# Optimization experiments

Hardware: AMD Instinct MI355X
Metric: run time of the kernel (lower is better)

Reference implementation:

```python
import jax, jax.numpy as jnp
import numpy as np

N = 100000      # nodes (max(content_indices)+1)
E = 1600000     # edges
TXT, VIS = 768, 512
IN = 128        # in_channels (already even)
FEAT = IN + 3   # feature_size = in_channels + 3 (ars)
HID, OUT, CAT = 128, 128, 2
NEG_SLOPE = 0.2


def setup_inputs() -> dict:
    key = jax.random.key(0)
    ks = jax.random.split(key, 20)
    p = lambda k, sh: jax.random.normal(k, sh, jnp.float32) * 0.02
    return {
        "image_features": jax.random.normal(ks[0], (N, VIS), jnp.float32),
        "text_features": jax.random.normal(ks[1], (N, TXT), jnp.float32),
        "content_indices": jnp.arange(N, dtype=jnp.int32),
        "gt_indices": jax.random.randint(ks[2], (N,), 0, 2, jnp.int32),
        "edges": jax.random.randint(ks[3], (E, 2), 0, N, jnp.int32),
        "ars": jax.random.uniform(ks[4], (N, 3), jnp.float32),
        # linear projections
        "Wi": p(ks[5], (VIS, IN // 2)), "bi": jnp.zeros((IN // 2,), jnp.float32),
        "Wt": p(ks[6], (TXT, IN // 2)), "bt": jnp.zeros((IN // 2,), jnp.float32),
        # GATConv layer 0: FEAT -> HID (heads=1)
        "W0": p(ks[7], (FEAT, HID)), "as0": p(ks[8], (HID,)), "ad0": p(ks[9], (HID,)),
        "b0": jnp.zeros((HID,), jnp.float32),
        # GATConv layer 1: HID -> OUT
        "W1": p(ks[10], (HID, OUT)), "as1": p(ks[11], (OUT,)), "ad1": p(ks[12], (OUT,)),
        "b1": jnp.zeros((OUT,), jnp.float32),
        "Wa": p(ks[13], (OUT, CAT)), "ba": jnp.zeros((CAT,), jnp.float32),
        "Wd": p(ks[14], (OUT, CAT)), "bd": jnp.zeros((CAT,), jnp.float32),
    }


def gat_conv(x, src, dst, W, att_src, att_dst, bias):
    """PyG GATConv, heads=1, add_self_loops=True, negative_slope=0.2."""
    h = x @ W                                    # [N, D]
    loop = jnp.arange(N, dtype=src.dtype)
    s = jnp.concatenate([src, loop])             # [E+N]
    d = jnp.concatenate([dst, loop])
    a_s = (h * att_src).sum(-1)                  # [N]
    a_d = (h * att_dst).sum(-1)
    e = jax.nn.leaky_relu(a_s[s] + a_d[d], NEG_SLOPE)   # [E+N]
    # segment softmax over incoming edges of each dst node
    e_max = jax.ops.segment_max(e, d, num_segments=N)
    ee = jnp.exp(e - e_max[d])
    denom = jax.ops.segment_sum(ee, d, num_segments=N)
    alpha = ee / (denom[d] + 1e-16)
    out = jax.ops.segment_sum(h[s] * alpha[:, None], d, num_segments=N)
    return out + bias


def reference(image_features, text_features, content_indices, gt_indices, edges, ars,
              Wi, bi, Wt, bt, W0, as0, ad0, b0, W1, as1, ad1, b1, Wa, ba, Wd, bd):
    img = image_features @ Wi + bi              # [N, IN//2]
    txt = text_features @ Wt + bt               # [N, IN//2]
    inp = jnp.concatenate([img, txt, ars], axis=1)   # [N, FEAT]
    node = jnp.zeros((N, FEAT), jnp.float32).at[content_indices].set(inp)
    node = jax.nn.gelu(node, approximate=False)
    src, dst = edges[:, 0], edges[:, 1]         # edge_index = edges.T
    h = gat_conv(node, src, dst, W0, as0, ad0, b0)
    h = jax.nn.relu(h)                          # PyG GAT inter-layer act
    h = gat_conv(h, src, dst, W1, as1, ad1, b1)
    out = jax.nn.gelu(h, approximate=False)     # [N, OUT]
    angles = out @ Wa + ba                      # [N, CAT]
    dists = out @ Wd + bd
    # per-edge tiny dot products (bmm of [E,1,C] x [E,C,1])
    ap = jnp.sum(angles[src] * angles[dst], axis=-1, keepdims=True)  # [E,1]
    dp = jnp.sum(dists[src] * dists[dst], axis=-1, keepdims=True)
    prediction = jnp.concatenate([ap, dp], axis=-1)   # [E, 2]
    return out, prediction
```

## Files before the change

kernel.cpp:

```cpp
#include <hip/hip_runtime.h>
#include <math.h>

#define N_NODES 100000
#define N_EDGES 1600000
#define FEAT 131
#define HID 128

__device__ __forceinline__ float geluf(float x) {
    return 0.5f * x * (1.0f + erff(x * 0.7071067811865475f));
}
__device__ __forceinline__ float leakyf(float x) {
    return x >= 0.0f ? x : 0.2f * x;
}
__device__ __forceinline__ float wave_reduce_max(float v) {
#pragma unroll
    for (int o = 32; o > 0; o >>= 1) v = fmaxf(v, __shfl_xor(v, o, 64));
    return v;
}
__device__ __forceinline__ float wave_reduce_sum(float v) {
#pragma unroll
    for (int o = 32; o > 0; o >>= 1) v += __shfl_xor(v, o, 64);
    return v;
}

template <int ACT>
__global__ __launch_bounds__(256) void gemm_tiled(
    const float* __restrict__ A, int lda, int M, int K,
    const float* __restrict__ B, int ldb,
    const float* __restrict__ bias,
    float* __restrict__ C, int ldc, int colOff,
    const int* __restrict__ rowIdx)
{
    __shared__ float As[16][68];
    __shared__ float Bs[16][64];
    int tid = threadIdx.x;
    int m0 = blockIdx.x * 64;
    int n0 = blockIdx.y * 64;
    int tx = tid & 15, ty = tid >> 4;
    float acc[4][4] = {};

    for (int k0 = 0; k0 < K; k0 += 16) {
#pragma unroll
        for (int i = 0; i < 4; ++i) {
            int idx = tid + i * 256;
            int r = idx >> 4, kk = idx & 15;
            int row = m0 + r, k = k0 + kk;
            As[kk][r] = (row < M && k < K) ? A[(size_t)row * lda + k] : 0.0f;
        }
#pragma unroll
        for (int i = 0; i < 4; ++i) {
            int idx = tid + i * 256;
            int kk = idx >> 6, c = idx & 63;
            int k = k0 + kk;
            Bs[kk][c] = (k < K) ? B[(size_t)k * ldb + n0 + c] : 0.0f;
        }
        __syncthreads();
#pragma unroll
        for (int kk = 0; kk < 16; ++kk) {
            float4 a4 = *(const float4*)&As[kk][ty * 4];
            float4 b4 = *(const float4*)&Bs[kk][tx * 4];
            float av[4] = {a4.x, a4.y, a4.z, a4.w};
            float bv[4] = {b4.x, b4.y, b4.z, b4.w};
#pragma unroll
            for (int i = 0; i < 4; ++i)
#pragma unroll
                for (int j = 0; j < 4; ++j)
                    acc[i][j] = fmaf(av[i], bv[j], acc[i][j]);
        }
        __syncthreads();
    }

#pragma unroll
    for (int i = 0; i < 4; ++i) {
        int row = m0 + ty * 4 + i;
        if (row >= M) continue;
        int orow = rowIdx ? rowIdx[row] : row;
#pragma unroll
        for (int j = 0; j < 4; ++j) {
            int c = n0 + tx * 4 + j;
            float v = acc[i][j];
            if (bias) v += bias[c];
            if (ACT == 1) v = geluf(v);
            C[(size_t)orow * ldc + colOff + c] = v;
        }
    }
}

__global__ void ars_kernel(const float* __restrict__ ars, const int* __restrict__ ci,
                           float* __restrict__ node)
{
    int i = blockIdx.x * blockDim.x + threadIdx.x;
    if (i >= N_NODES * 3) return;
    int n = i / 3, j = i - n * 3;
    node[(size_t)ci[n] * FEAT + 128 + j] = geluf(ars[i]);
}

__global__ void hist_dst(const int* __restrict__ edges, int* __restrict__ deg)
{
    int e = blockIdx.x * blockDim.x + threadIdx.x;
    if (e < N_EDGES) atomicAdd(&deg[edges[2 * e + 1]], 1);
}

__global__ __launch_bounds__(1024) void scan_excl(const int* __restrict__ deg,
                                                  int* __restrict__ row_ptr)
{
    __shared__ int sd[1024];
    int tid = threadIdx.x;
    int base = 0;
    for (int start = 0; start < N_NODES; start += 1024) {
        int i = start + tid;
        int v = (i < N_NODES) ? deg[i] : 0;
        sd[tid] = v;
        __syncthreads();
        for (int off = 1; off < 1024; off <<= 1) {
            int t = (tid >= off) ? sd[tid - off] : 0;
            __syncthreads();
            sd[tid] += t;
            __syncthreads();
        }
        if (i < N_NODES) row_ptr[i] = base + sd[tid] - v;
        base += sd[1023];
        __syncthreads();
    }
    if (tid == 0) row_ptr[N_NODES] = base;
}

__global__ void copy_int(const int* __restrict__ src, int* __restrict__ dst, int n)
{
    int i = blockIdx.x * blockDim.x + threadIdx.x;
    if (i < n) dst[i] = src[i];
}

__global__ void scatter_csr(const int* __restrict__ edges, int* __restrict__ cursor,
                            int* __restrict__ csr_src)
{
    int e = blockIdx.x * blockDim.x + threadIdx.x;
    if (e >= N_EDGES) return;
    int s = edges[2 * e], d = edges[2 * e + 1];
    int pos = atomicAdd(&cursor[d], 1);
    csr_src[pos] = s;
}

__global__ __launch_bounds__(256) void attn_scores(
    const float* __restrict__ h, const float* __restrict__ atts,
    const float* __restrict__ attd, float* __restrict__ as_, float* __restrict__ ad_)
{
    int lane = threadIdx.x & 63;
    int node = blockIdx.x * 4 + (threadIdx.x >> 6);
    if (node >= N_NODES) return;
    float h0 = h[(size_t)node * HID + lane];
    float h1 = h[(size_t)node * HID + 64 + lane];
    float s = h0 * atts[lane] + h1 * atts[64 + lane];
    float d = h0 * attd[lane] + h1 * attd[64 + lane];
    s = wave_reduce_sum(s);
    d = wave_reduce_sum(d);
    if (lane == 0) { as_[node] = s; ad_[node] = d; }
}

template <int ACT>
__global__ __launch_bounds__(256) void gat_aggregate(
    const float* __restrict__ h,
    const float* __restrict__ as_, const float* __restrict__ ad_,
    const int* __restrict__ row_ptr, const int* __restrict__ csr_src,
    const float* __restrict__ bias, float* __restrict__ outp)
{
    int lane = threadIdx.x & 63;
    int node = blockIdx.x * 4 + (threadIdx.x >> 6);
    if (node >= N_NODES) return;
    int start = row_ptr[node];
    int deg = row_ptr[node + 1] - start;
    float adn = ad_[node];
    float e_self = leakyf(as_[node] + adn);
    float acc0 = 0.0f, acc1 = 0.0f;
    float m, denom;

    if (deg <= 64) {
        int s = 0;
        float e = -INFINITY;
        if (lane < deg) {
            s = csr_src[start + lane];
            e = leakyf(as_[s] + adn);
        }
        m = fmaxf(wave_reduce_max(e), e_self);
        float w = (lane < deg) ? __expf(e - m) : 0.0f;
        denom = wave_reduce_sum(w) + __expf(e_self - m);
        for (int jj = 0; jj < deg; ++jj) {
            int sj = __shfl(s, jj, 64);
            float wj = __shfl(w, jj, 64);
            acc0 += wj * h[(size_t)sj * HID + lane];
            acc1 += wj * h[(size_t)sj * HID + 64 + lane];
        }
    } else {
        float lm = -INFINITY;
        for (int j = lane; j < deg; j += 64)
            lm = fmaxf(lm, leakyf(as_[csr_src[start + j]] + adn));
        m = fmaxf(wave_reduce_max(lm), e_self);
        float lsum = 0.0f;
        for (int j = lane; j < deg; j += 64)
            lsum += __expf(leakyf(as_[csr_src[start + j]] + adn) - m);
        denom = wave_reduce_sum(lsum) + __expf(e_self - m);
        for (int c0 = 0; c0 < deg; c0 += 64) {
            int j = c0 + lane;
            int s = 0;
            float w = 0.0f;
            if (j < deg) {
                s = csr_src[start + j];
                w = __expf(leakyf(as_[s] + adn) - m);
            }
            int cnt = min(64, deg - c0);
            for (int jj = 0; jj < cnt; ++jj) {
                int sj = __shfl(s, jj, 64);
                float wj = __shfl(w, jj, 64);
                acc0 += wj * h[(size_t)sj * HID + lane];
                acc1 += wj * h[(size_t)sj * HID + 64 + lane];
            }
        }
    }

    float wself = __expf(e_self - m);
    acc0 = (acc0 + wself * h[(size_t)node * HID + lane]) / denom;
    acc1 = (acc1 + wself * h[(size_t)node * HID + 64 + lane]) / denom;
    acc0 += bias[lane];
    acc1 += bias[64 + lane];
    if (ACT == 0) {
        acc0 = fmaxf(acc0, 0.0f);
        acc1 = fmaxf(acc1, 0.0f);
    } else {
        acc0 = geluf(acc0);
        acc1 = geluf(acc1);
    }
    outp[(size_t)node * HID + lane] = acc0;
    outp[(size_t)node * HID + 64 + lane] = acc1;
}

__global__ __launch_bounds__(256) void head_proj(
    const float* __restrict__ outf,
    const float* __restrict__ Wa, const float* __restrict__ ba,
    const float* __restrict__ Wd, const float* __restrict__ bd,
    float* __restrict__ adp)
{
    int lane = threadIdx.x & 63;
    int node = blockIdx.x * 4 + (threadIdx.x >> 6);
    if (node >= N_NODES) return;
    float o0 = outf[(size_t)node * HID + lane];
    float o1 = outf[(size_t)node * HID + 64 + lane];
    float a0 = o0 * Wa[lane * 2] + o1 * Wa[(lane + 64) * 2];
    float a1 = o0 * Wa[lane * 2 + 1] + o1 * Wa[(lane + 64) * 2 + 1];
    float d0 = o0 * Wd[lane * 2] + o1 * Wd[(lane + 64) * 2];
    float d1 = o0 * Wd[lane * 2 + 1] + o1 * Wd[(lane + 64) * 2 + 1];
    a0 = wave_reduce_sum(a0);
    a1 = wave_reduce_sum(a1);
    d0 = wave_reduce_sum(d0);
    d1 = wave_reduce_sum(d1);
    if (lane == 0) {
        float4 v = make_float4(a0 + ba[0], a1 + ba[1], d0 + bd[0], d1 + bd[1]);
        ((float4*)adp)[node] = v;
    }
}

__global__ void edge_pred(const int* __restrict__ edges, const float* __restrict__ adp,
                          float* __restrict__ pred)
{
    int e = blockIdx.x * blockDim.x + threadIdx.x;
    if (e >= N_EDGES) return;
    int s = edges[2 * e], d = edges[2 * e + 1];
    float4 ps = ((const float4*)adp)[s];
    float4 pd = ((const float4*)adp)[d];
    pred[2 * e] = ps.x * pd.x + ps.y * pd.y;
    pred[2 * e + 1] = ps.z * pd.z + ps.w * pd.w;
}

extern "C" void kernel_launch(void* const* d_in, const int* in_sizes, int n_in,
                              void* d_out, int out_size, void* d_ws, size_t ws_size,
                              hipStream_t stream)
{
    const float* imgf = (const float*)d_in[0];
    const float* txtf = (const float*)d_in[1];
    const int* ci     = (const int*)d_in[2];
    const int* edges  = (const int*)d_in[4];
    const float* ars  = (const float*)d_in[5];
    const float* Wi   = (const float*)d_in[6];
    const float* bi   = (const float*)d_in[7];
    const float* Wt   = (const float*)d_in[8];
    const float* bt   = (const float*)d_in[9];
    const float* W0   = (const float*)d_in[10];
    const float* as0  = (const float*)d_in[11];
    const float* ad0  = (const float*)d_in[12];
    const float* b0   = (const float*)d_in[13];
    const float* W1   = (const float*)d_in[14];
    const float* as1  = (const float*)d_in[15];
    const float* ad1  = (const float*)d_in[16];
    const float* b1   = (const float*)d_in[17];
    const float* Wa   = (const float*)d_in[18];
    const float* ba   = (const float*)d_in[19];
    const float* Wd   = (const float*)d_in[20];
    const float* bd   = (const float*)d_in[21];
    (void)in_sizes; (void)n_in; (void)out_size; (void)ws_size;

    float* out0 = (float*)d_out;
    float* pred = out0 + (size_t)N_NODES * HID;

    char* ws = (char*)d_ws;
    size_t off = 0;
    auto alloc = [&](size_t bytes) -> void* {
        void* p = ws + off;
        off += (bytes + 255) & ~(size_t)255;
        return p;
    };
    float* node   = (float*)alloc((size_t)N_NODES * FEAT * 4);
    float* hA     = (float*)alloc((size_t)N_NODES * HID * 4);
    float* as_buf = (float*)alloc((size_t)N_NODES * 4);
    float* ad_buf = (float*)alloc((size_t)N_NODES * 4);
    int* row_ptr  = (int*)alloc((size_t)(N_NODES + 1) * 4);
    int* cursor   = (int*)alloc((size_t)N_NODES * 4);
    int* csr_src  = (int*)alloc((size_t)N_EDGES * 4);
    float* adp    = (float*)alloc((size_t)N_NODES * 4 * 4);

    int mtiles = (N_NODES + 63) / 64;
    int nwaveblocks = N_NODES / 4;

    hipMemsetAsync(cursor, 0, (size_t)N_NODES * 4, stream);
    hist_dst<<<(N_EDGES + 255) / 256, 256, 0, stream>>>(edges, cursor);
    scan_excl<<<1, 1024, 0, stream>>>(cursor, row_ptr);
    copy_int<<<(N_NODES + 255) / 256, 256, 0, stream>>>(row_ptr, cursor, N_NODES);
    scatter_csr<<<(N_EDGES + 255) / 256, 256, 0, stream>>>(edges, cursor, csr_src);

    gemm_tiled<1><<<dim3(mtiles, 1), 256, 0, stream>>>(imgf, 512, N_NODES, 512, Wi, 64, bi, node, FEAT, 0, ci);
    gemm_tiled<1><<<dim3(mtiles, 1), 256, 0, stream>>>(txtf, 768, N_NODES, 768, Wt, 64, bt, node, FEAT, 64, ci);
    ars_kernel<<<(N_NODES * 3 + 255) / 256, 256, 0, stream>>>(ars, ci, node);

    gemm_tiled<0><<<dim3(mtiles, 2), 256, 0, stream>>>(node, FEAT, N_NODES, FEAT, W0, HID, nullptr, hA, HID, 0, nullptr);
    attn_scores<<<nwaveblocks, 256, 0, stream>>>(hA, as0, ad0, as_buf, ad_buf);
    gat_aggregate<0><<<nwaveblocks, 256, 0, stream>>>(hA, as_buf, ad_buf, row_ptr, csr_src, b0, node);

    gemm_tiled<0><<<dim3(mtiles, 2), 256, 0, stream>>>(node, HID, N_NODES, HID, W1, HID, nullptr, hA, HID, 0, nullptr);
    attn_scores<<<nwaveblocks, 256, 0, stream>>>(hA, as1, ad1, as_buf, ad_buf);
    gat_aggregate<1><<<nwaveblocks, 256, 0, stream>>>(hA, as_buf, ad_buf, row_ptr, csr_src, b1, out0);

    head_proj<<<nwaveblocks, 256, 0, stream>>>(out0, Wa, ba, Wd, bd, adp);
    edge_pred<<<(N_EDGES + 255) / 256, 256, 0, stream>>>(edges, adp, pred);
}
```

Before: 1.835 ms.

## Use 128x64 register-prefetched GEMM tiles with float4 loads and padded features

Replaces the 64x64 GEMM with a 128x64 tile that computes 8x4 outputs per thread over a K-step of 32. It prefetches the next global tile into registers while the current one is computed, and uses float4 loads and stores. The node feature width is padded from 131 to 132, and W0 is zero-padded to match, so rows are 16-byte aligned for vector access. In exchange it uses more registers and shared memory per block and adds a small padding kernel.

```diff
diff --git a/kernel.cpp b/kernel.cpp
--- a/kernel.cpp
+++ b/kernel.cpp
@@ -3,7 +3,7 @@
 
 #define N_NODES 100000
 #define N_EDGES 1600000
-#define FEAT 131
+#define FEATP 132
 #define HID 128
 
 __device__ __forceinline__ float geluf(float x) {
@@ -24,45 +24,69 @@
 }
 
 template <int ACT>
-__global__ __launch_bounds__(256) void gemm_tiled(
+__global__ __launch_bounds__(256) void gemm128(
     const float* __restrict__ A, int lda, int M, int K,
     const float* __restrict__ B, int ldb,
     const float* __restrict__ bias,
     float* __restrict__ C, int ldc, int colOff,
     const int* __restrict__ rowIdx)
 {
-    __shared__ float As[16][68];
-    __shared__ float Bs[16][64];
-    int tid = threadIdx.x;
-    int m0 = blockIdx.x * 64;
-    int n0 = blockIdx.y * 64;
-    int tx = tid & 15, ty = tid >> 4;
-    float acc[4][4] = {};
-
-    for (int k0 = 0; k0 < K; k0 += 16) {
+    __shared__ float As[32][132];
+    __shared__ float Bs[32][64];
+    const int tid = threadIdx.x;
+    const int m0 = blockIdx.x * 128;
+    const int n0 = blockIdx.y * 64;
+    const int tx = tid & 15, ty = tid >> 4;
+
+    const int arow = tid >> 3;
+    const int acol = (tid & 7) * 4;
+    const int brow = tid >> 4;
+    const int bcol = (tid & 15) * 4;
+
+    float4 pa[4], pb[2];
+    const int T = (K + 31) / 32;
+
+    auto fetch = [&](int k0) {
 #pragma unroll
         for (int i = 0; i < 4; ++i) {
-            int idx = tid + i * 256;
-            int r = idx >> 4, kk = idx & 15;
-            int row = m0 + r, k = k0 + kk;
-            As[kk][r] = (row < M && k < K) ? A[(size_t)row * lda + k] : 0.0f;
-        }
+            int row = m0 + i * 32 + arow;
+            int k = k0 + acol;
+            pa[i] = (row < M && k < K) ? *(const float4*)&A[(size_t)row * lda + k]
+                                       : make_float4(0.f, 0.f, 0.f, 0.f);
+        }
+#pragma unroll
+        for (int i = 0; i < 2; ++i) {
+            int k = k0 + i * 16 + brow;
+            pb[i] = (k < K) ? *(const float4*)&B[(size_t)k * ldb + n0 + bcol]
+                            : make_float4(0.f, 0.f, 0.f, 0.f);
+        }
+    };
+
+    float acc[8][4] = {};
+    fetch(0);
+    for (int t = 0; t < T; ++t) {
 #pragma unroll
         for (int i = 0; i < 4; ++i) {
-            int idx = tid + i * 256;
-            int kk = idx >> 6, c = idx & 63;
-            int k = k0 + kk;
-            Bs[kk][c] = (k < K) ? B[(size_t)k * ldb + n0 + c] : 0.0f;
-        }
+            int row = i * 32 + arow;
+            As[acol + 0][row] = pa[i].x;
+            As[acol + 1][row] = pa[i].y;
+            As[acol + 2][row] = pa[i].z;
+            As[acol + 3][row] = pa[i].w;
+        }
+#pragma unroll
+        for (int i = 0; i < 2; ++i)
+            *(float4*)&Bs[i * 16 + brow][bcol] = pb[i];
         __syncthreads();
-#pragma unroll
-        for (int kk = 0; kk < 16; ++kk) {
-            float4 a4 = *(const float4*)&As[kk][ty * 4];
-            float4 b4 = *(const float4*)&Bs[kk][tx * 4];
-            float av[4] = {a4.x, a4.y, a4.z, a4.w};
-            float bv[4] = {b4.x, b4.y, b4.z, b4.w};
-#pragma unroll
-            for (int i = 0; i < 4; ++i)
+        if (t + 1 < T) fetch((t + 1) * 32);
+#pragma unroll
+        for (int kk = 0; kk < 32; ++kk) {
+            float4 a0 = *(const float4*)&As[kk][ty * 8];
+            float4 a1 = *(const float4*)&As[kk][ty * 8 + 4];
+            float4 b  = *(const float4*)&Bs[kk][tx * 4];
+            float av[8] = {a0.x, a0.y, a0.z, a0.w, a1.x, a1.y, a1.z, a1.w};
+            float bv[4] = {b.x, b.y, b.z, b.w};
+#pragma unroll
+            for (int i = 0; i < 8; ++i)
 #pragma unroll
                 for (int j = 0; j < 4; ++j)
                     acc[i][j] = fmaf(av[i], bv[j], acc[i][j]);
@@ -71,18 +95,20 @@
     }
 
 #pragma unroll
-    for (int i = 0; i < 4; ++i) {
-        int row = m0 + ty * 4 + i;
+    for (int i = 0; i < 8; ++i) {
+        int row = m0 + ty * 8 + i;
         if (row >= M) continue;
         int orow = rowIdx ? rowIdx[row] : row;
+        float4 v;
+        float* vp = (float*)&v;
 #pragma unroll
         for (int j = 0; j < 4; ++j) {
-            int c = n0 + tx * 4 + j;
-            float v = acc[i][j];
-            if (bias) v += bias[c];
-            if (ACT == 1) v = geluf(v);
-            C[(size_t)orow * ldc + colOff + c] = v;
-        }
+            float x = acc[i][j];
+            if (bias) x += bias[n0 + tx * 4 + j];
+            if (ACT == 1) x = geluf(x);
+            vp[j] = x;
+        }
+        *(float4*)&C[(size_t)orow * ldc + colOff + n0 + tx * 4] = v;
     }
 }
 
@@ -90,9 +116,18 @@
                            float* __restrict__ node)
 {
     int i = blockIdx.x * blockDim.x + threadIdx.x;
-    if (i >= N_NODES * 3) return;
-    int n = i / 3, j = i - n * 3;
-    node[(size_t)ci[n] * FEAT + 128 + j] = geluf(ars[i]);
+    if (i >= N_NODES * 4) return;
+    int n = i >> 2, j = i & 3;
+    float v = (j < 3) ? geluf(ars[n * 3 + j]) : 0.0f;
+    node[(size_t)ci[n] * FEATP + 128 + j] = v;
+}
+
+__global__ void pad_W0(const float* __restrict__ W0, float* __restrict__ W0p)
+{
+    int i = blockIdx.x * blockDim.x + threadIdx.x;
+    if (i >= FEATP * HID) return;
+    int r = i >> 7;
+    W0p[i] = (r < 131) ? W0[i] : 0.0f;
 }
 
 __global__ void hist_dst(const int* __restrict__ edges, int* __restrict__ deg)
@@ -307,7 +342,7 @@
         off += (bytes + 255) & ~(size_t)255;
         return p;
     };
-    float* node   = (float*)alloc((size_t)N_NODES * FEAT * 4);
+    float* node   = (float*)alloc((size_t)N_NODES * FEATP * 4);
     float* hA     = (float*)alloc((size_t)N_NODES * HID * 4);
     float* as_buf = (float*)alloc((size_t)N_NODES * 4);
     float* ad_buf = (float*)alloc((size_t)N_NODES * 4);
@@ -315,8 +350,9 @@
     int* cursor   = (int*)alloc((size_t)N_NODES * 4);
     int* csr_src  = (int*)alloc((size_t)N_EDGES * 4);
     float* adp    = (float*)alloc((size_t)N_NODES * 4 * 4);
-
-    int mtiles = (N_NODES + 63) / 64;
+    float* W0p    = (float*)alloc((size_t)FEATP * HID * 4);
+
+    int mtiles = (N_NODES + 127) / 128;
     int nwaveblocks = N_NODES / 4;
 
     hipMemsetAsync(cursor, 0, (size_t)N_NODES * 4, stream);
@@ -324,16 +360,17 @@
     scan_excl<<<1, 1024, 0, stream>>>(cursor, row_ptr);
     copy_int<<<(N_NODES + 255) / 256, 256, 0, stream>>>(row_ptr, cursor, N_NODES);
     scatter_csr<<<(N_EDGES + 255) / 256, 256, 0, stream>>>(edges, cursor, csr_src);
-
-    gemm_tiled<1><<<dim3(mtiles, 1), 256, 0, stream>>>(imgf, 512, N_NODES, 512, Wi, 64, bi, node, FEAT, 0, ci);
-    gemm_tiled<1><<<dim3(mtiles, 1), 256, 0, stream>>>(txtf, 768, N_NODES, 768, Wt, 64, bt, node, FEAT, 64, ci);
-    ars_kernel<<<(N_NODES * 3 + 255) / 256, 256, 0, stream>>>(ars, ci, node);
-
-    gemm_tiled<0><<<dim3(mtiles, 2), 256, 0, stream>>>(node, FEAT, N_NODES, FEAT, W0, HID, nullptr, hA, HID, 0, nullptr);
+    pad_W0<<<(FEATP * HID + 255) / 256, 256, 0, stream>>>(W0, W0p);
+
+    gemm128<1><<<dim3(mtiles, 1), 256, 0, stream>>>(imgf, 512, N_NODES, 512, Wi, 64, bi, node, FEATP, 0, ci);
+    gemm128<1><<<dim3(mtiles, 1), 256, 0, stream>>>(txtf, 768, N_NODES, 768, Wt, 64, bt, node, FEATP, 64, ci);
+    ars_kernel<<<(N_NODES * 4 + 255) / 256, 256, 0, stream>>>(ars, ci, node);
+
+    gemm128<0><<<dim3(mtiles, 2), 256, 0, stream>>>(node, FEATP, N_NODES, FEATP, W0p, HID, nullptr, hA, HID, 0, nullptr);
     attn_scores<<<nwaveblocks, 256, 0, stream>>>(hA, as0, ad0, as_buf, ad_buf);
     gat_aggregate<0><<<nwaveblocks, 256, 0, stream>>>(hA, as_buf, ad_buf, row_ptr, csr_src, b0, node);
 
-    gemm_tiled<0><<<dim3(mtiles, 2), 256, 0, stream>>>(node, HID, N_NODES, HID, W1, HID, nullptr, hA, HID, 0, nullptr);
+    gemm128<0><<<dim3(mtiles, 2), 256, 0, stream>>>(node, HID, N_NODES, HID, W1, HID, nullptr, hA, HID, 0, nullptr);
     attn_scores<<<nwaveblocks, 256, 0, stream>>>(hA, as1, ad1, as_buf, ad_buf);
     gat_aggregate<1><<<nwaveblocks, 256, 0, stream>>>(hA, as_buf, ad_buf, row_ptr, csr_src, b1, out0);
 
```

Result: faster. 1.589 ms (-13.4%).
